# Kernel optimization log

Hardware: AMD Instinct MI355X
Metric: run time of the kernel (lower is better)

Reference implementation:

```python
import jax, jax.numpy as jnp
import numpy as np

B, C, H, Wd = 4, 144, 64, 64
CM = 64          # mid channels (planes[1..3])
K, PAD = 5, 2    # proj_kernel_size unfold
EPS = 1e-5       # BatchNorm eps


def _bn(x, g, b, m, v, axis=1):
    sh = [1] * x.ndim
    sh[axis] = -1
    return (x - m.reshape(sh)) * (g.reshape(sh) * jax.lax.rsqrt(v.reshape(sh) + EPS)) + b.reshape(sh)


def setup_inputs():
    key = jax.random.key(0)
    ks = jax.random.split(key, 24)
    def w(k, shape, s=0.1):
        return jax.random.normal(k, shape, dtype=jnp.float32) * s
    inp = {
        'x': jax.random.normal(ks[0], (B, C, H, Wd), dtype=jnp.float32),
        'w_in': w(ks[1], (CM, C)),
        'g_in': 1.0 + w(ks[2], (CM,)), 'b_in': w(ks[3], (CM,)),
        'm_in': w(ks[4], (CM,)), 'v_in': jax.random.uniform(ks[5], (CM,), minval=0.5, maxval=1.5),
        'w1': w(ks[6], (CM, CM, 3, 3)),
        'g1': 1.0 + w(ks[7], (CM,)), 'b1': w(ks[8], (CM,)),
        'm1': w(ks[9], (CM,)), 'v1': jax.random.uniform(ks[10], (CM,), minval=0.5, maxval=1.5),
        'w2': w(ks[11], (CM, CM, 3, 3)),
        'g2': 1.0 + w(ks[12], (CM,)), 'b2': w(ks[13], (CM,)),
        'm2': w(ks[14], (CM,)), 'v2': jax.random.uniform(ks[15], (CM,), minval=0.5, maxval=1.5),
        'w_out': w(ks[16], (C, CM)),
        'g_out': 1.0 + w(ks[17], (C,)), 'b_out': w(ks[18], (C,)),
        'm_out': w(ks[19], (C,)), 'v_out': jax.random.uniform(ks[20], (C,), minval=0.5, maxval=1.5),
    }
    return inp


def _forward(x, w_in, g_in, b_in, m_in, v_in, w1, g1, b1, m1, v1,
             w2, g2, b2, m2, v2, w_out, g_out, b_out, m_out, v_out):
    b, c, h, wd = x.shape
    # F.normalize over channel dim (L2, eps=1e-12)
    x = x / jnp.maximum(jnp.sqrt(jnp.sum(x * x, axis=1, keepdims=True)), 1e-12)
    # 5x5 unfold (im2col), pad 2 -> patches [b, c, K*K, h, w] (row-major (kh,kw) like torch)
    xp = jnp.pad(x, ((0, 0), (0, 0), (PAD, PAD), (PAD, PAD)))
    patches = jnp.stack([xp[:, :, i:i + h, j:j + wd]
                         for i in range(K) for j in range(K)], axis=2)
    # elementwise correlation with center pixel, reorder -> [b, c, h*w, K*K]
    y = patches * x[:, :, None, :, :]
    y = jnp.moveaxis(y, 2, -1).reshape(b, c, h * wd, K * K)
    # conv1x1_in + BN + ReLU (1x1 conv == channel matmul)
    z = jnp.einsum('oc,bcpk->bopk', w_in, y)
    z = jax.nn.relu(_bn(z, g_in, b_in, m_in, v_in, axis=1))
    cm = z.shape[1]
    # Conv3d kernel (1,3,3) VALID == 2D 3x3 conv per spatial position: fold h*w into batch
    z = z.reshape(b, cm, h * wd, K, K).transpose(0, 2, 1, 3, 4).reshape(b * h * wd, cm, K, K)
    dn = ('NCHW', 'OIHW', 'NCHW')
    z = jax.lax.conv_general_dilated(z, w1, (1, 1), 'VALID', dimension_numbers=dn)
    z = jax.nn.relu(_bn(z, g1, b1, m1, v1, axis=1))  # [b*hw, cm, 3, 3]
    z = jax.lax.conv_general_dilated(z, w2, (1, 1), 'VALID', dimension_numbers=dn)
    z = jax.nn.relu(_bn(z, g2, b2, m2, v2, axis=1))  # [b*hw, cm, 1, 1]
    z = z.reshape(b, h * wd, cm).transpose(0, 2, 1).reshape(b, cm, h, wd)
    # conv1x1_out + BN (final layer: no ReLU)
    out = jnp.einsum('oc,bchw->bohw', w_out, z)
    return _bn(out, g_out, b_out, m_out, v_out, axis=1)


def reference(x, w_in, g_in, b_in, m_in, v_in, w1, g1, b1, m1, v1,
              w2, g2, b2, m2, v2, w_out, g_out, b_out, m_out, v_out):
    return _forward(x, w_in, g_in, b_in, m_in, v_in, w1, g1, b1, m1, v1,
                    w2, g2, b2, m2, v2, w_out, g_out, b_out, m_out, v_out)
```

## Files before the change

### kernel.cpp

```cpp
#include <hip/hip_runtime.h>

#define BB   4
#define CC   144
#define HW   4096
#define PTOT 16384
#define EPSB 1e-5f

typedef __bf16 bf16;
typedef __bf16 bf16x8 __attribute__((ext_vector_type(8)));
typedef float  f32x4  __attribute__((ext_vector_type(4)));
typedef unsigned short U16;
typedef U16 u16x4 __attribute__((ext_vector_type(4)));
typedef U16 u16x8 __attribute__((ext_vector_type(8)));

#define MFMA __builtin_amdgcn_mfma_f32_16x16x32_bf16

#define XN_OFF    0UL
#define WINF_OFF  76021760UL
#define W1F_OFF   76042240UL
#define W2F_OFF   76115968UL
#define WOUTF_OFF 76189696UL
#define BNP_OFF   76208128UL

__global__ __launch_bounds__(576) void k_norm(const float* __restrict__ x,
                                              bf16* __restrict__ xn2)
{
    __shared__ float red[9][64];
    int bh = blockIdx.x;
    int t = threadIdx.x, w = t & 63, cq = t >> 6;
    const float* px = x + ((size_t)(bh >> 6) * CC) * HW + (bh & 63) * 64 + w;
    float vals[16];
    float s = 0.f;
    #pragma unroll
    for (int i = 0; i < 16; i++) {
        float v = px[(size_t)(cq * 16 + i) * HW];
        vals[i] = v; s += v * v;
    }
    red[cq][w] = s;
    __syncthreads();
    float tot = 0.f;
    #pragma unroll
    for (int q = 0; q < 9; q++) tot += red[q][w];
    float inv = 1.f / fmaxf(sqrtf(tot), 1e-12f);
    size_t p = (size_t)bh * 64 + w;
    #pragma unroll
    for (int k = 0; k < 2; k++) {
        int g = cq * 2 + k;
        u16x8 pk;
        #pragma unroll
        for (int j = 0; j < 8; j++) {
            bf16 v = (bf16)(vals[k * 8 + j] * inv);
            pk[j] = *(U16*)&v;
        }
        *(u16x8*)(xn2 + (((size_t)g) << 17) + p * 8) = pk;
    }
}

__global__ __launch_bounds__(256) void k_pack(
    const float* __restrict__ w_in, const float* __restrict__ w1,
    const float* __restrict__ w2,   const float* __restrict__ w_out,
    const float* g_in, const float* b_in, const float* m_in, const float* v_in,
    const float* g1,   const float* b1,   const float* m1,   const float* v1,
    const float* g2,   const float* b2,   const float* m2,   const float* v2,
    const float* g_out,const float* b_out,const float* m_out,const float* v_out,
    bf16* w_inf, bf16* w1f, bf16* w2f, bf16* w_outf, float* bnp)
{
    int t = blockIdx.x * 256 + threadIdx.x;
    if (t < 10240) {
        int e = t, j = e & 7, lane = (e >> 3) & 63, r = e >> 9;
        int ks = r % 5, mt = r / 5;
        int o = mt * 16 + (lane & 15);
        int c = ks * 32 + ((lane >> 4) << 3) + j;
        float s = g_in[o] * rsqrtf(v_in[o] + EPSB);
        w_inf[e] = (c < 144) ? (bf16)(w_in[o * 144 + c] * s) : (bf16)0.f;
    } else if (t < 47104) {
        int e = t - 10240, j = e & 7, lane = (e >> 3) & 63, r = e >> 9;
        int ks = r % 18, mt = r / 18;
        int o = mt * 16 + (lane & 15);
        int k = ks * 32 + ((lane >> 4) << 3) + j;
        int ij = k >> 6, c = k & 63;
        float s = g1[o] * rsqrtf(v1[o] + EPSB);
        w1f[e] = (bf16)(w1[(o * 64 + c) * 9 + ij] * s);
    } else if (t < 83968) {
        int e = t - 47104, j = e & 7, lane = (e >> 3) & 63, r = e >> 9;
        int ks = r % 18, mt = r / 18;
        int o = mt * 16 + (lane & 15);
        int k = ks * 32 + ((lane >> 4) << 3) + j;
        int rs = k >> 6, c2 = k & 63;
        float s = g2[o] * rsqrtf(v2[o] + EPSB);
        w2f[e] = (bf16)(w2[o * 576 + c2 * 9 + rs] * s);
    } else if (t < 93184) {
        int e = t - 83968, j = e & 7, lane = (e >> 3) & 63, r = e >> 9;
        int ks = r & 1, mt = r >> 1;
        int o = mt * 16 + (lane & 15);
        int c = ks * 32 + ((lane >> 4) << 3) + j;
        float s = g_out[o] * rsqrtf(v_out[o] + EPSB);
        w_outf[e] = (bf16)(w_out[o * 64 + c] * s);
    } else if (t < 93856) {
        int i = t - 93184;
        const float *g, *bb, *mm, *vv; int c; bool is_t;
        if (i < 128)      { g=g_in; bb=b_in; mm=m_in; vv=v_in; c=i&63;        is_t=i>=64;  }
        else if (i < 256) { g=g1;   bb=b1;   mm=m1;   vv=v1;   c=(i-128)&63;  is_t=i>=192; }
        else if (i < 384) { g=g2;   bb=b2;   mm=m2;   vv=v2;   c=(i-256)&63;  is_t=i>=320; }
        else              { int ii=i-384; g=g_out; bb=b_out; mm=m_out; vv=v_out;
                            c = ii % 144; is_t = ii >= 144; }
        float s = g[c] * rsqrtf(vv[c] + EPSB);
        bnp[i] = is_t ? (bb[c] - mm[c] * s) : s;
    }
}

__global__ __launch_bounds__(256, 2) void k_fused(const bf16* __restrict__ xn2,
        const bf16* __restrict__ w_inf, const bf16* __restrict__ w1f,
        const bf16* __restrict__ w2f,   const bf16* __restrict__ w_outf,
        const float* __restrict__ bnp,  float* __restrict__ out)
{
    __shared__ __align__(16) U16 lds[25600];
    U16* a2_lds = lds;
    U16* v3     = lds + 9216;

    const int LUT5c[9] = {0, 1, 2, 5, 6, 7, 10, 11, 12};

    int t = threadIdx.x, wid = t >> 6, lane = t & 63;
    int quad = lane >> 4, pl = lane & 15;
    int raw = blockIdx.x;
    int bid = (raw & 7) * 128 + (raw >> 3);
    int p0 = bid * 16;
    int b = p0 >> 12, h = (p0 >> 6) & 63, w0 = p0 & 63, hw0 = p0 & 4095;
    int wc = w0 + pl;

    bf16x8 af[4][5];
    #pragma unroll
    for (int mt = 0; mt < 4; mt++)
        #pragma unroll
        for (int ks = 0; ks < 5; ks++)
            af[mt][ks] = *(const bf16x8*)(w_inf + ((mt * 5 + ks) * 64 + lane) * 8);
    bf16x8 cfr[5];
    #pragma unroll
    for (int ks = 0; ks < 5; ks++) {
        int g = ks * 4 + quad;
        bf16x8 z = {};
        cfr[ks] = (g < 18) ? *(const bf16x8*)(xn2 + ((size_t)g << 17) + (size_t)(p0 + pl) * 8) : z;
    }
    f32x4 tv[4];
    #pragma unroll
    for (int mt = 0; mt < 4; mt++)
        tv[mt] = *(const f32x4*)&bnp[64 + mt * 16 + quad * 4];

    for (int kp = wid; kp < 25; kp += 4) {
        int kpr = kp / 5, kpc = kp - kpr * 5;
        int dh = kpr - 2, dw = kpc - 2;
        bool ok = ((unsigned)(h + dh) < 64u) && ((unsigned)(wc + dw) < 64u);
        size_t pn = (size_t)(p0 + dh * 64 + dw + pl);
        f32x4 acc[4] = {};
        #pragma unroll
        for (int ks = 0; ks < 5; ks++) {
            int g = ks * 4 + quad;
            bf16x8 nv = {};
            if (ok && g < 18)
                nv = *(const bf16x8*)(xn2 + ((size_t)g << 17) + pn * 8);
            bf16x8 bfr;
            #pragma unroll
            for (int j = 0; j < 8; j++)
                bfr[j] = (bf16)((float)nv[j] * (float)cfr[ks][j]);
            #pragma unroll
            for (int mt = 0; mt < 4; mt++)
                acc[mt] = MFMA(af[mt][ks], bfr, acc[mt], 0, 0, 0);
        }
        int swb = kp * 3 + pl;
        #pragma unroll
        for (int mt = 0; mt < 4; mt++) {
            u16x4 pk;
            #pragma unroll
            for (int r = 0; r < 4; r++) {
                bf16 v = (bf16)fmaxf(acc[mt][r] + tv[mt][r], 0.f);
                pk[r] = *(U16*)&v;
            }
            int g0 = mt * 2 + (quad >> 1);
            int dst = pl * 1600 + kp * 64 + (((g0 + swb) & 7) << 3) + (quad & 1) * 4;
            *(u16x4*)&lds[dst] = pk;
        }
    }
    __syncthreads();

    int mhalf = wid & 1, rsh = wid >> 1;
    int NR = 5 - rsh;
    const int L5E[5] = {0, 2, 6, 10, 12};
    const int L5O[5] = {1, 5, 7, 11, 11};
    f32x4 acc2[5][2] = {};
    #pragma unroll
    for (int ks = 0; ks < 18; ks++) {
        int ij = ks >> 1;
        bf16x8 aa0 = *(const bf16x8*)(w1f + (((mhalf * 2 + 0) * 18 + ks) * 64 + lane) * 8);
        bf16x8 aa1 = *(const bf16x8*)(w1f + (((mhalf * 2 + 1) * 18 + ks) * 64 + lane) * 8);
        int gb = (ks & 1) * 4 + quad;
        int l5ij = LUT5c[ij];
        #pragma unroll
        for (int i = 0; i < 5; i++) {
            if (i < NR) {
                int l5rs = rsh ? L5O[i] : L5E[i];
                int kpidx = l5ij + l5rs;
                int off = pl * 1600 + kpidx * 64 + (((gb + kpidx * 3 + pl) & 7) << 3);
                bf16x8 bfr = *(const bf16x8*)&lds[off];
                acc2[i][0] = MFMA(aa0, bfr, acc2[i][0], 0, 0, 0);
                acc2[i][1] = MFMA(aa1, bfr, acc2[i][1], 0, 0, 0);
            }
        }
    }
    f32x4 t1v[2];
    #pragma unroll
    for (int m = 0; m < 2; m++)
        t1v[m] = *(const f32x4*)&bnp[192 + (mhalf * 2 + m) * 16 + quad * 4];
    u16x4 pk2[5][2];
    #pragma unroll
    for (int i = 0; i < 5; i++) {
        if (i < NR) {
            #pragma unroll
            for (int m = 0; m < 2; m++) {
                #pragma unroll
                for (int r = 0; r < 4; r++) {
                    bf16 v = (bf16)fmaxf(acc2[i][m][r] + t1v[m][r], 0.f);
                    pk2[i][m][r] = *(U16*)&v;
                }
            }
        }
    }
    __syncthreads();
    #pragma unroll
    for (int i = 0; i < 5; i++) {
        if (i < NR) {
            int rs = 2 * i + rsh;
            #pragma unroll
            for (int m = 0; m < 2; m++) {
                int mb = mhalf * 2 + m;
                int c = rs * 8 + mb * 2 + (quad >> 1);
                int dst = pl * 576 + ((c >> 3) << 6) + ((((c & 7) + pl) & 7) << 3) + (quad & 1) * 4;
                *(u16x4*)&a2_lds[dst] = pk2[i][m];
            }
        }
    }
    __syncthreads();

    {
        int mt = wid;
        f32x4 acc3 = {};
        #pragma unroll
        for (int ks = 0; ks < 18; ks++) {
            bf16x8 afr = *(const bf16x8*)(w2f + ((mt * 18 + ks) * 64 + lane) * 8);
            int cg = ks * 4 + quad;
            int off = pl * 576 + ((cg >> 3) << 6) + ((((cg & 7) + pl) & 7) << 3);
            bf16x8 bfr = *(const bf16x8*)&a2_lds[off];
            acc3 = MFMA(afr, bfr, acc3, 0, 0, 0);
        }
        #pragma unroll
        for (int r = 0; r < 4; r++) {
            int o = mt * 16 + quad * 4 + r;
            bf16 yb = (bf16)fmaxf(acc3[r] + bnp[320 + o], 0.f);
            v3[pl * 64 + ((((o >> 3) + pl) & 7) << 3) + (o & 7)] = *(U16*)&yb;
        }
    }
    __syncthreads();

    for (int mt = wid; mt < 9; mt += 4) {
        f32x4 accB = {};
        #pragma unroll
        for (int ks = 0; ks < 2; ks++) {
            bf16x8 afr = *(const bf16x8*)(w_outf + ((mt * 2 + ks) * 64 + lane) * 8);
            int g = ks * 4 + quad;
            bf16x8 bfr = *(const bf16x8*)&v3[pl * 64 + (((g + pl) & 7) << 3)];
            accB = MFMA(afr, bfr, accB, 0, 0, 0);
        }
        #pragma unroll
        for (int r = 0; r < 4; r++) {
            int oc = mt * 16 + quad * 4 + r;
            out[((size_t)(b * 144 + oc)) * 4096 + hw0 + pl] = accB[r] + bnp[528 + oc];
        }
    }
}

extern "C" void kernel_launch(void* const* d_in, const int* in_sizes, int n_in,
                              void* d_out, int out_size, void* d_ws, size_t ws_size,
                              hipStream_t stream)
{
    const float* x     = (const float*)d_in[0];
    const float* w_in  = (const float*)d_in[1];
    const float* g_in  = (const float*)d_in[2];
    const float* b_in  = (const float*)d_in[3];
    const float* m_in  = (const float*)d_in[4];
    const float* v_in  = (const float*)d_in[5];
    const float* w1    = (const float*)d_in[6];
    const float* g1    = (const float*)d_in[7];
    const float* b1    = (const float*)d_in[8];
    const float* m1    = (const float*)d_in[9];
    const float* v1    = (const float*)d_in[10];
    const float* w2    = (const float*)d_in[11];
    const float* g2    = (const float*)d_in[12];
    const float* b2    = (const float*)d_in[13];
    const float* m2    = (const float*)d_in[14];
    const float* v2    = (const float*)d_in[15];
    const float* w_out = (const float*)d_in[16];
    const float* g_out = (const float*)d_in[17];
    const float* b_out = (const float*)d_in[18];
    const float* m_out = (const float*)d_in[19];
    const float* v_out = (const float*)d_in[20];
    float* out = (float*)d_out;

    char* ws = (char*)d_ws;
    bf16*  xn2    = (bf16*)(ws + XN_OFF);
    bf16*  w_inf  = (bf16*)(ws + WINF_OFF);
    bf16*  w1f    = (bf16*)(ws + W1F_OFF);
    bf16*  w2f    = (bf16*)(ws + W2F_OFF);
    bf16*  w_outf = (bf16*)(ws + WOUTF_OFF);
    float* bnp    = (float*)(ws + BNP_OFF);

    hipLaunchKernelGGL(k_norm, dim3(256), dim3(576), 0, stream, x, xn2);
    hipLaunchKernelGGL(k_pack, dim3(367), dim3(256), 0, stream,
                       w_in, w1, w2, w_out,
                       g_in, b_in, m_in, v_in, g1, b1, m1, v1,
                       g2, b2, m2, v2, g_out, b_out, m_out, v_out,
                       w_inf, w1f, w2f, w_outf, bnp);
    hipLaunchKernelGGL(k_fused, dim3(1024), dim3(256), 0, stream,
                       xn2, w_inf, w1f, w2f, w_outf, bnp, out);
}
```

Measured before the change: 147.4 us.

## Merge prep kernels, repartition 3x3 conv work per wave, prefetch weights

The normalization and weight-packing kernels become one launch, removing a kernel boundary. In the fused kernel, the first 3x3 conv stage gives each wave one 16-channel output tile across all nine positions instead of the previous split by half-channels and row subsets. Neighbour loads in stage one are batched ahead of the MFMAs, weight fragments are double-buffered for both 3x3 stages, and the launch bound asks for three blocks per CU. Together these aim to cut launch overhead, balance work across waves and hide latency, but nine accumulators plus nine B fragments raise register pressure, which can conflict with the higher occupancy target and cause spills.

Result: slower. 155.2 us (+5.3%).

```diff
diff --git a/kernel.cpp b/kernel.cpp
--- a/kernel.cpp
+++ b/kernel.cpp
@@ -22,50 +22,48 @@
 #define WOUTF_OFF 76189696UL
 #define BNP_OFF   76208128UL
 
-__global__ __launch_bounds__(576) void k_norm(const float* __restrict__ x,
-                                              bf16* __restrict__ xn2)
-{
-    __shared__ float red[9][64];
-    int bh = blockIdx.x;
-    int t = threadIdx.x, w = t & 63, cq = t >> 6;
-    const float* px = x + ((size_t)(bh >> 6) * CC) * HW + (bh & 63) * 64 + w;
-    float vals[16];
-    float s = 0.f;
-    #pragma unroll
-    for (int i = 0; i < 16; i++) {
-        float v = px[(size_t)(cq * 16 + i) * HW];
-        vals[i] = v; s += v * v;
-    }
-    red[cq][w] = s;
-    __syncthreads();
-    float tot = 0.f;
-    #pragma unroll
-    for (int q = 0; q < 9; q++) tot += red[q][w];
-    float inv = 1.f / fmaxf(sqrtf(tot), 1e-12f);
-    size_t p = (size_t)bh * 64 + w;
-    #pragma unroll
-    for (int k = 0; k < 2; k++) {
-        int g = cq * 2 + k;
-        u16x8 pk;
-        #pragma unroll
-        for (int j = 0; j < 8; j++) {
-            bf16 v = (bf16)(vals[k * 8 + j] * inv);
-            pk[j] = *(U16*)&v;
-        }
-        *(u16x8*)(xn2 + (((size_t)g) << 17) + p * 8) = pk;
-    }
-}
-
-__global__ __launch_bounds__(256) void k_pack(
+__global__ __launch_bounds__(576) void k_prep(const float* __restrict__ x,
     const float* __restrict__ w_in, const float* __restrict__ w1,
     const float* __restrict__ w2,   const float* __restrict__ w_out,
     const float* g_in, const float* b_in, const float* m_in, const float* v_in,
     const float* g1,   const float* b1,   const float* m1,   const float* v1,
     const float* g2,   const float* b2,   const float* m2,   const float* v2,
     const float* g_out,const float* b_out,const float* m_out,const float* v_out,
-    bf16* w_inf, bf16* w1f, bf16* w2f, bf16* w_outf, float* bnp)
+    bf16* xn2, bf16* w_inf, bf16* w1f, bf16* w2f, bf16* w_outf, float* bnp)
 {
-    int t = blockIdx.x * 256 + threadIdx.x;
+    __shared__ float red[9][64];
+    if (blockIdx.x < 256) {
+        int bh = blockIdx.x;
+        int t = threadIdx.x, w = t & 63, cq = t >> 6;
+        const float* px = x + ((size_t)(bh >> 6) * CC) * HW + (bh & 63) * 64 + w;
+        float vals[16];
+        float s = 0.f;
+        #pragma unroll
+        for (int i = 0; i < 16; i++) {
+            float v = px[(size_t)(cq * 16 + i) * HW];
+            vals[i] = v; s += v * v;
+        }
+        red[cq][w] = s;
+        __syncthreads();
+        float tot = 0.f;
+        #pragma unroll
+        for (int q = 0; q < 9; q++) tot += red[q][w];
+        float inv = 1.f / fmaxf(sqrtf(tot), 1e-12f);
+        size_t p = (size_t)bh * 64 + w;
+        #pragma unroll
+        for (int k = 0; k < 2; k++) {
+            int g = cq * 2 + k;
+            u16x8 pk;
+            #pragma unroll
+            for (int j = 0; j < 8; j++) {
+                bf16 v = (bf16)(vals[k * 8 + j] * inv);
+                pk[j] = *(U16*)&v;
+            }
+            *(u16x8*)(xn2 + (((size_t)g) << 17) + p * 8) = pk;
+        }
+        return;
+    }
+    int t = (blockIdx.x - 256) * 576 + threadIdx.x;
     if (t < 10240) {
         int e = t, j = e & 7, lane = (e >> 3) & 63, r = e >> 9;
         int ks = r % 5, mt = r / 5;
@@ -109,7 +107,7 @@
     }
 }
 
-__global__ __launch_bounds__(256, 2) void k_fused(const bf16* __restrict__ xn2,
+__global__ __launch_bounds__(256, 3) void k_fused(const bf16* __restrict__ xn2,
         const bf16* __restrict__ w_inf, const bf16* __restrict__ w1f,
         const bf16* __restrict__ w2f,   const bf16* __restrict__ w_outf,
         const float* __restrict__ bnp,  float* __restrict__ out)
@@ -125,8 +123,8 @@
     int raw = blockIdx.x;
     int bid = (raw & 7) * 128 + (raw >> 3);
     int p0 = bid * 16;
-    int b = p0 >> 12, h = (p0 >> 6) & 63, w0 = p0 & 63, hw0 = p0 & 4095;
-    int wc = w0 + pl;
+    int b = p0 >> 12, h = (p0 >> 6) & 63, hw0 = p0 & 4095;
+    int wc = (p0 & 63) + pl;
 
     bf16x8 af[4][5];
     #pragma unroll
@@ -151,17 +149,20 @@
         int dh = kpr - 2, dw = kpc - 2;
         bool ok = ((unsigned)(h + dh) < 64u) && ((unsigned)(wc + dw) < 64u);
         size_t pn = (size_t)(p0 + dh * 64 + dw + pl);
-        f32x4 acc[4] = {};
+        bf16x8 nv[5];
         #pragma unroll
         for (int ks = 0; ks < 5; ks++) {
             int g = ks * 4 + quad;
-            bf16x8 nv = {};
-            if (ok && g < 18)
-                nv = *(const bf16x8*)(xn2 + ((size_t)g << 17) + pn * 8);
+            bf16x8 z = {};
+            nv[ks] = (ok && g < 18) ? *(const bf16x8*)(xn2 + ((size_t)g << 17) + pn * 8) : z;
+        }
+        f32x4 acc[4] = {};
+        #pragma unroll
+        for (int ks = 0; ks < 5; ks++) {
             bf16x8 bfr;
             #pragma unroll
             for (int j = 0; j < 8; j++)
-                bfr[j] = (bf16)((float)nv[j] * (float)cfr[ks][j]);
+                bfr[j] = (bf16)((float)nv[ks][j] * (float)cfr[ks][j]);
             #pragma unroll
             for (int mt = 0; mt < 4; mt++)
                 acc[mt] = MFMA(af[mt][ks], bfr, acc[mt], 0, 0, 0);
@@ -182,60 +183,44 @@
     }
     __syncthreads();
 
-    int mhalf = wid & 1, rsh = wid >> 1;
-    int NR = 5 - rsh;
-    const int L5E[5] = {0, 2, 6, 10, 12};
-    const int L5O[5] = {1, 5, 7, 11, 11};
-    f32x4 acc2[5][2] = {};
-    #pragma unroll
-    for (int ks = 0; ks < 18; ks++) {
-        int ij = ks >> 1;
-        bf16x8 aa0 = *(const bf16x8*)(w1f + (((mhalf * 2 + 0) * 18 + ks) * 64 + lane) * 8);
-        bf16x8 aa1 = *(const bf16x8*)(w1f + (((mhalf * 2 + 1) * 18 + ks) * 64 + lane) * 8);
-        int gb = (ks & 1) * 4 + quad;
-        int l5ij = LUT5c[ij];
-        #pragma unroll
-        for (int i = 0; i < 5; i++) {
-            if (i < NR) {
-                int l5rs = rsh ? L5O[i] : L5E[i];
-                int kpidx = l5ij + l5rs;
+    {
+        int mt = wid;
+        f32x4 acc2[9] = {};
+        bf16x8 aaC[2];
+        aaC[0] = *(const bf16x8*)(w1f + ((mt * 18 + 0) * 64 + lane) * 8);
+        #pragma unroll
+        for (int ks = 0; ks < 18; ks++) {
+            if (ks + 1 < 18)
+                aaC[(ks + 1) & 1] = *(const bf16x8*)(w1f + ((mt * 18 + ks + 1) * 64 + lane) * 8);
+            int ij = ks >> 1, gb = (ks & 1) * 4 + quad;
+            int l5 = LUT5c[ij];
+            bf16x8 bfr[9];
+            #pragma unroll
+            for (int rs = 0; rs < 9; rs++) {
+                int kpidx = l5 + LUT5c[rs];
                 int off = pl * 1600 + kpidx * 64 + (((gb + kpidx * 3 + pl) & 7) << 3);
-                bf16x8 bfr = *(const bf16x8*)&lds[off];
-                acc2[i][0] = MFMA(aa0, bfr, acc2[i][0], 0, 0, 0);
-                acc2[i][1] = MFMA(aa1, bfr, acc2[i][1], 0, 0, 0);
+                bfr[rs] = *(const bf16x8*)&lds[off];
             }
-        }
-    }
-    f32x4 t1v[2];
-    #pragma unroll
-    for (int m = 0; m < 2; m++)
-        t1v[m] = *(const f32x4*)&bnp[192 + (mhalf * 2 + m) * 16 + quad * 4];
-    u16x4 pk2[5][2];
-    #pragma unroll
-    for (int i = 0; i < 5; i++) {
-        if (i < NR) {
-            #pragma unroll
-            for (int m = 0; m < 2; m++) {
-                #pragma unroll
-                for (int r = 0; r < 4; r++) {
-                    bf16 v = (bf16)fmaxf(acc2[i][m][r] + t1v[m][r], 0.f);
-                    pk2[i][m][r] = *(U16*)&v;
-                }
+            #pragma unroll
+            for (int rs = 0; rs < 9; rs++)
+                acc2[rs] = MFMA(aaC[ks & 1], bfr[rs], acc2[rs], 0, 0, 0);
+        }
+        f32x4 t1v = *(const f32x4*)&bnp[192 + mt * 16 + quad * 4];
+        u16x4 pk2[9];
+        #pragma unroll
+        for (int rs = 0; rs < 9; rs++) {
+            #pragma unroll
+            for (int r = 0; r < 4; r++) {
+                bf16 v = (bf16)fmaxf(acc2[rs][r] + t1v[r], 0.f);
+                pk2[rs][r] = *(U16*)&v;
             }
         }
-    }
-    __syncthreads();
-    #pragma unroll
-    for (int i = 0; i < 5; i++) {
-        if (i < NR) {
-            int rs = 2 * i + rsh;
-            #pragma unroll
-            for (int m = 0; m < 2; m++) {
-                int mb = mhalf * 2 + m;
-                int c = rs * 8 + mb * 2 + (quad >> 1);
-                int dst = pl * 576 + ((c >> 3) << 6) + ((((c & 7) + pl) & 7) << 3) + (quad & 1) * 4;
-                *(u16x4*)&a2_lds[dst] = pk2[i][m];
-            }
+        __syncthreads();
+        #pragma unroll
+        for (int rs = 0; rs < 9; rs++) {
+            int c = rs * 8 + mt * 2 + (quad >> 1);
+            int dst = pl * 576 + ((c >> 3) << 6) + ((((c & 7) + pl) & 7) << 3) + (quad & 1) * 4;
+            *(u16x4*)&a2_lds[dst] = pk2[rs];
         }
     }
     __syncthreads();
@@ -243,13 +228,16 @@
     {
         int mt = wid;
         f32x4 acc3 = {};
+        bf16x8 aaD[2];
+        aaD[0] = *(const bf16x8*)(w2f + ((mt * 18 + 0) * 64 + lane) * 8);
         #pragma unroll
         for (int ks = 0; ks < 18; ks++) {
-            bf16x8 afr = *(const bf16x8*)(w2f + ((mt * 18 + ks) * 64 + lane) * 8);
+            if (ks + 1 < 18)
+                aaD[(ks + 1) & 1] = *(const bf16x8*)(w2f + ((mt * 18 + ks + 1) * 64 + lane) * 8);
             int cg = ks * 4 + quad;
             int off = pl * 576 + ((cg >> 3) << 6) + ((((cg & 7) + pl) & 7) << 3);
             bf16x8 bfr = *(const bf16x8*)&a2_lds[off];
-            acc3 = MFMA(afr, bfr, acc3, 0, 0, 0);
+            acc3 = MFMA(aaD[ks & 1], bfr, acc3, 0, 0, 0);
         }
         #pragma unroll
         for (int r = 0; r < 4; r++) {
@@ -261,14 +249,13 @@
     __syncthreads();
 
     for (int mt = wid; mt < 9; mt += 4) {
+        bf16x8 afr0 = *(const bf16x8*)(w_outf + ((mt * 2 + 0) * 64 + lane) * 8);
+        bf16x8 afr1 = *(const bf16x8*)(w_outf + ((mt * 2 + 1) * 64 + lane) * 8);
+        bf16x8 bfr0 = *(const bf16x8*)&v3[pl * 64 + ((((0 * 4 + quad) + pl) & 7) << 3)];
+        bf16x8 bfr1 = *(const bf16x8*)&v3[pl * 64 + ((((1 * 4 + quad) + pl) & 7) << 3)];
         f32x4 accB = {};
-        #pragma unroll
-        for (int ks = 0; ks < 2; ks++) {
-            bf16x8 afr = *(const bf16x8*)(w_outf + ((mt * 2 + ks) * 64 + lane) * 8);
-            int g = ks * 4 + quad;
-            bf16x8 bfr = *(const bf16x8*)&v3[pl * 64 + (((g + pl) & 7) << 3)];
-            accB = MFMA(afr, bfr, accB, 0, 0, 0);
-        }
+        accB = MFMA(afr0, bfr0, accB, 0, 0, 0);
+        accB = MFMA(afr1, bfr1, accB, 0, 0, 0);
         #pragma unroll
         for (int r = 0; r < 4; r++) {
             int oc = mt * 16 + quad * 4 + r;
@@ -312,12 +299,11 @@
     bf16*  w_outf = (bf16*)(ws + WOUTF_OFF);
     float* bnp    = (float*)(ws + BNP_OFF);
 
-    hipLaunchKernelGGL(k_norm, dim3(256), dim3(576), 0, stream, x, xn2);
-    hipLaunchKernelGGL(k_pack, dim3(367), dim3(256), 0, stream,
-                       w_in, w1, w2, w_out,
+    hipLaunchKernelGGL(k_prep, dim3(419), dim3(576), 0, stream,
+                       x, w_in, w1, w2, w_out,
                        g_in, b_in, m_in, v_in, g1, b1, m1, v1,
                        g2, b2, m2, v2, g_out, b_out, m_out, v_out,
-                       w_inf, w1f, w2f, w_outf, bnp);
+                       xn2, w_inf, w1f, w2f, w_outf, bnp);
     hipLaunchKernelGGL(k_fused, dim3(1024), dim3(256), 0, stream,
                        xn2, w_inf, w1f, w2f, w_outf, bnp, out);
 }
```
